# Optimization experiments

Hardware: AMD Instinct MI355X
Metric: run time of the kernel (lower is better)

The kernel has to match this reference:

```python
import jax, jax.numpy as jnp
import numpy as np

D_MODEL = 1024
NUM_HEADS = 16
D_K = D_MODEL // NUM_HEADS
B, S = 1, 4096


def setup_inputs() -> dict:
    key = jax.random.key(0)
    ks = jax.random.split(key, 11)
    std = 1.0 / np.sqrt(D_MODEL)
    def lin(k):
        kw, kb = jax.random.split(k)
        W = jax.random.uniform(kw, (D_MODEL, D_MODEL), jnp.float32, -std, std)
        b = jax.random.uniform(kb, (D_MODEL,), jnp.float32, -std, std)
        return W, b
    Wq, bq = lin(ks[0]); Wk, bk = lin(ks[1]); Wv, bv = lin(ks[2]); Wo, bo = lin(ks[3])
    q = jax.random.normal(ks[4], (B, S, D_MODEL), jnp.float32)
    k = jax.random.normal(ks[5], (B, S, D_MODEL), jnp.float32)
    v = jax.random.normal(ks[6], (B, S, D_MODEL), jnp.float32)
    return {"q": q, "k": k, "v": v,
            "Wq": Wq, "bq": bq, "Wk": Wk, "bk": bk,
            "Wv": Wv, "bv": bv, "Wo": Wo, "bo": bo}


def reference(q, k, v, Wq, bq, Wk, bk, Wv, bv, Wo, bo):
    Bq, Sq, _ = q.shape
    # Linear projections (torch Linear: x @ W.T + b)
    def split_heads(x):
        return x.reshape(Bq, -1, NUM_HEADS, D_K).transpose(0, 2, 1, 3)  # [B,H,S,Dk]
    query = split_heads(q @ Wq.T + bq)
    key_ = split_heads(k @ Wk.T + bk)
    value = split_heads(v @ Wv.T + bv)
    scores = jnp.einsum('bhsd,bhtd->bhst', query, key_) / jnp.sqrt(jnp.float32(D_K))
    attn = jax.nn.softmax(scores, axis=-1)  # [B,H,S,S]
    ctx = jnp.einsum('bhst,bhtd->bhsd', attn, value)
    ctx = ctx.transpose(0, 2, 1, 3).reshape(Bq, Sq, NUM_HEADS * D_K)
    return ctx @ Wo.T + bo
```

## Files before the change

kernel.cpp:

```cpp
#include <hip/hip_runtime.h>
#include <cstdint>
#include <cstddef>

#define S_LEN 4096
#define DMODEL 1024
#define NHEADS 16
#define DK 64
#define ACT (S_LEN * DMODEL)
#define WELE (DMODEL * DMODEL)

typedef __bf16 bf16;
typedef bf16  bf16x2 __attribute__((ext_vector_type(2)));
typedef bf16  bf16x4 __attribute__((ext_vector_type(4)));
typedef bf16  bf16x8 __attribute__((ext_vector_type(8)));
typedef float f32x4  __attribute__((ext_vector_type(4)));
typedef float f32x16 __attribute__((ext_vector_type(16)));
typedef unsigned int uint32x4v __attribute__((ext_vector_type(4)));

__device__ __forceinline__ void async16(const void* g, void* l) {
    __builtin_amdgcn_global_load_lds(
        (__attribute__((address_space(1))) void*)(uintptr_t)g,
        (__attribute__((address_space(3))) void*)(uintptr_t)l,
        16, 0, 0);
}

__device__ __forceinline__ float fast_exp2(float x) {
#if __has_builtin(__builtin_amdgcn_exp2f)
    return __builtin_amdgcn_exp2f(x);
#else
    return exp2f(x);
#endif
}

__device__ __forceinline__ unsigned pk2(float a, float b) {
    bf16x2 t; t[0] = (bf16)a; t[1] = (bf16)b;
    return __builtin_bit_cast(unsigned, t);
}

__device__ __forceinline__ void pl32swap(unsigned &a, unsigned &b) {
    asm volatile("v_permlane32_swap_b32 %0, %1" : "+v"(a), "+v"(b));
}

__device__ __forceinline__ bf16x8 mkfrag(unsigned w0, unsigned w1, unsigned w2, unsigned w3) {
    uint32x4v u = { w0, w1, w2, w3 };
    return __builtin_bit_cast(bf16x8, u);
}

__global__ void __launch_bounds__(256) cvt7(
    const float* a0, const float* a1, const float* a2,
    const float* w0, const float* w1, const float* w2, const float* w3,
    bf16* oa0, bf16* oa1, bf16* oa2,
    bf16* ow0, bf16* ow1, bf16* ow2, bf16* ow3,
    int nA, int nB)
{
    const float* s; bf16* d; int n4;
    switch (blockIdx.y) {
        case 0: s = a0; d = oa0; n4 = nA; break;
        case 1: s = a1; d = oa1; n4 = nA; break;
        case 2: s = a2; d = oa2; n4 = nA; break;
        case 3: s = w0; d = ow0; n4 = nB; break;
        case 4: s = w1; d = ow1; n4 = nB; break;
        case 5: s = w2; d = ow2; n4 = nB; break;
        default: s = w3; d = ow3; n4 = nB; break;
    }
    int i = blockIdx.x * 256 + threadIdx.x;
    if (i < n4) {
        float4 v = ((const float4*)s)[i];
        bf16x4 r = { (bf16)v.x, (bf16)v.y, (bf16)v.z, (bf16)v.w };
        ((bf16x4*)d)[i] = r;
    }
}

__device__ __forceinline__ void gemm_compute_128(
    const bf16* As, const bf16* Bs, f32x4 (&acc)[4][4],
    int wm, int wn, int l16, int quad)
{
    bf16x8 af[4], bfr[4];
#pragma unroll
    for (int i = 0; i < 4; ++i)
        af[i] = *(const bf16x8*)&As[(wm + i * 16 + l16) * 32 + quad * 8];
#pragma unroll
    for (int i = 0; i < 4; ++i)
        bfr[i] = *(const bf16x8*)&Bs[(wn + i * 16 + l16) * 32 + quad * 8];
#pragma unroll
    for (int mi = 0; mi < 4; ++mi)
#pragma unroll
        for (int ni = 0; ni < 4; ++ni)
            acc[mi][ni] = __builtin_amdgcn_mfma_f32_16x16x32_bf16(
                af[mi], bfr[ni], acc[mi][ni], 0, 0, 0);
}

__device__ __forceinline__ void gemm_core_bk64(
    const bf16* __restrict__ A, const bf16* __restrict__ B,
    bf16* As, bf16* Bs, f32x4 (&acc)[4][4],
    int m0, int n0, int wm, int wn, int K)
{
    const int tid  = threadIdx.x;
    const int wave = tid >> 6;
    const int lane = tid & 63;
    const int quad = lane >> 4;
    const int l16  = lane & 15;

    const int srow = tid >> 2;
    const int scol = (tid & 3) * 8;
    const bf16* Ag = A + (size_t)(m0 + srow) * K + scol;
    const bf16* Bg = B + (size_t)(n0 + srow) * K + scol;
    char* lA = (char*)As + wave * 1024;
    char* lB = (char*)Bs + wave * 1024;

    for (int k0 = 0; k0 < K; k0 += 64) {
        async16(Ag,                       lA);
        async16(Ag + (size_t)64 * K,      lA + 4096);
        async16(Ag + 32,                  lA + 8192);
        async16(Ag + 32 + (size_t)64 * K, lA + 12288);
        async16(Bg,                       lB);
        async16(Bg + (size_t)64 * K,      lB + 4096);
        async16(Bg + 32,                  lB + 8192);
        async16(Bg + 32 + (size_t)64 * K, lB + 12288);
        Ag += 64; Bg += 64;
        __syncthreads();

        gemm_compute_128(As,        Bs,        acc, wm, wn, l16, quad);
        gemm_compute_128(As + 4096, Bs + 4096, acc, wm, wn, l16, quad);
        __syncthreads();
    }
}

__global__ void __launch_bounds__(256) proj_qkv(
    const bf16* __restrict__ Xq, const bf16* __restrict__ Wq, const float* __restrict__ bq, bf16* __restrict__ Qo,
    const bf16* __restrict__ Xk, const bf16* __restrict__ Wk, const float* __restrict__ bk, bf16* __restrict__ Ko,
    const bf16* __restrict__ Xv, const bf16* __restrict__ Wv, const float* __restrict__ bv, bf16* __restrict__ Vo,
    float qscale)
{
    __shared__ __align__(16) bf16 As[2 * 128 * 32];
    __shared__ __align__(16) bf16 Bs[2 * 128 * 32];

    const int which = blockIdx.z;
    const bf16*  A    = (which == 0) ? Xq : (which == 1) ? Xk : Xv;
    const bf16*  Bw   = (which == 0) ? Wq : (which == 1) ? Wk : Wv;
    const float* bias = (which == 0) ? bq : (which == 1) ? bk : bv;
    const float  scale = (which == 0) ? qscale : 1.0f;

    const int tid  = threadIdx.x;
    const int wave = tid >> 6;
    const int lane = tid & 63;
    const int quad = lane >> 4;
    const int l16  = lane & 15;
    const int m0 = blockIdx.x * 128;
    const int n0 = blockIdx.y * 128;
    const int wm = (wave & 1) * 64;
    const int wn = (wave >> 1) * 64;

    f32x4 acc[4][4] = {};
    gemm_core_bk64(A, Bw, As, Bs, acc, m0, n0, wm, wn, DMODEL);

    if (which < 2) {
        bf16* out = (which == 0) ? Qo : Ko;
#pragma unroll
        for (int mi = 0; mi < 4; ++mi)
#pragma unroll
            for (int ni = 0; ni < 4; ++ni) {
                const int n = n0 + wn + ni * 16 + l16;
                const float bn = bias[n];
                const int dk = n & 63;
                const int cc = dk >> 3, ee = dk & 7;
                const size_t hb = (size_t)(n >> 6) * S_LEN * DK;
#pragma unroll
                for (int r = 0; r < 4; ++r) {
                    const int m = m0 + wm + mi * 16 + quad * 4 + r;
                    const int pdk = ((cc ^ (m & 7)) << 3) | ee;
                    out[hb + (size_t)m * DK + pdk] = (bf16)((acc[mi][ni][r] + bn) * scale);
                }
            }
    } else {
#pragma unroll
        for (int mi = 0; mi < 4; ++mi)
#pragma unroll
            for (int ni = 0; ni < 4; ++ni) {
                const int n = n0 + wn + ni * 16 + l16;
                const float bn = bias[n];
                const int dk = n & 63;
                const size_t hb = (size_t)(n >> 6) * (64 * S_LEN);
                const int mbase = m0 + wm + mi * 16 + quad * 4;
                const int T  = mbase >> 6;
                const int tt = mbase & 63;
                const int pos = (((tt >> 3) ^ (dk & 7)) << 3) | (tt & 7);
                bf16x4 r4;
#pragma unroll
                for (int r = 0; r < 4; ++r) r4[r] = (bf16)(acc[mi][ni][r] + bn);
                *(bf16x4*)&Vo[hb + (size_t)T * 4096 + dk * 64 + pos] = r4;
            }
    }
}

__global__ void __launch_bounds__(256) gemm_out(
    const bf16* __restrict__ A, const bf16* __restrict__ Bw,
    const float* __restrict__ bias, float* __restrict__ out)
{
    __shared__ __align__(16) bf16 As[64 * 32];
    __shared__ __align__(16) bf16 Bs[128 * 32];

    const int tid  = threadIdx.x;
    const int wave = tid >> 6;
    const int lane = tid & 63;
    const int quad = lane >> 4;
    const int l16  = lane & 15;
    const int m0 = blockIdx.x * 64;
    const int n0 = blockIdx.y * 128;
    const int wm = (wave & 1) * 32;
    const int wn = (wave >> 1) * 64;

    const int srow = tid >> 2;
    const int scol = (tid & 3) * 8;
    const bf16* Ag  = A  + (size_t)(m0 + srow) * DMODEL + scol;
    const bf16* Bg  = Bw + (size_t)(n0 + srow) * DMODEL + scol;
    const bf16* Bg2 = Bg + (size_t)64 * DMODEL;

    f32x4 acc[2][4] = {};
    for (int k0 = 0; k0 < DMODEL; k0 += 32) {
        async16(Ag,  (char*)As + wave * 1024);
        async16(Bg,  (char*)Bs + wave * 1024);
        async16(Bg2, (char*)Bs + 4096 + wave * 1024);
        Ag += 32; Bg += 32; Bg2 += 32;
        __syncthreads();

        bf16x8 af[2], bfr[4];
#pragma unroll
        for (int i = 0; i < 2; ++i)
            af[i] = *(const bf16x8*)&As[(wm + i * 16 + l16) * 32 + quad * 8];
#pragma unroll
        for (int i = 0; i < 4; ++i)
            bfr[i] = *(const bf16x8*)&Bs[(wn + i * 16 + l16) * 32 + quad * 8];

#pragma unroll
        for (int mi = 0; mi < 2; ++mi)
#pragma unroll
            for (int ni = 0; ni < 4; ++ni)
                acc[mi][ni] = __builtin_amdgcn_mfma_f32_16x16x32_bf16(
                    af[mi], bfr[ni], acc[mi][ni], 0, 0, 0);
        __syncthreads();
    }

#pragma unroll
    for (int mi = 0; mi < 2; ++mi)
#pragma unroll
        for (int ni = 0; ni < 4; ++ni) {
            const int n = n0 + wn + ni * 16 + l16;
            const float bn = bias[n];
#pragma unroll
            for (int r = 0; r < 4; ++r) {
                const int m = m0 + wm + mi * 16 + quad * 4 + r;
                out[(size_t)m * DMODEL + n] = acc[mi][ni][r] + bn;
            }
        }
}

__global__ void __launch_bounds__(512) flash_attn(
    const bf16* __restrict__ Q, const bf16* __restrict__ Kh,
    const bf16* __restrict__ Vt, bf16* __restrict__ ctx)
{
    __shared__ __align__(16) bf16 Qs[256 * 64];
    __shared__ __align__(16) bf16 Ks[3][64 * 64];
    __shared__ __align__(16) bf16 Vs[3][64 * 64];

    const int tid  = threadIdx.x;
    const int wave = tid >> 6;
    const int lane = tid & 63;
    const int l31  = lane & 31;
    const int hi   = lane >> 5;
    const int x7   = lane & 7;
    const int s0 = blockIdx.x * 256;
    const int h  = blockIdx.y;

    const bf16* Kg = Kh + (size_t)h * S_LEN * DK + tid * 8;
    const bf16* Vg = Vt + (size_t)h * (64 * S_LEN) + tid * 8;

    {
        const bf16* Qg = Q + (size_t)h * S_LEN * DK + (size_t)s0 * DK + tid * 8;
#pragma unroll
        for (int j = 0; j < 4; ++j)
            async16(Qg + j * 4096, (char*)Qs + j * 8192 + wave * 1024);
    }
    async16(Kg, (char*)Ks + wave * 1024);
    async16(Vg, (char*)Vs + wave * 1024);
    Kg += 4096; Vg += 4096;
    async16(Kg, (char*)Ks + 8192 + wave * 1024);
    async16(Vg, (char*)Vs + 8192 + wave * 1024);
    Kg += 4096; Vg += 4096;
    asm volatile("s_waitcnt vmcnt(2)" ::: "memory");
    __builtin_amdgcn_s_barrier();
    __builtin_amdgcn_sched_barrier(0);

    bf16x8 qf[4];
    {
        const bf16* qb = &Qs[(wave * 32 + l31) * 64];
#pragma unroll
        for (int ks = 0; ks < 4; ++ks)
            qf[ks] = *(const bf16x8*)(qb + ((((ks << 1) + hi) ^ x7) << 3));
    }

    f32x16 od[2] = {};
    float lsum = 0.0f;

    auto compute = [&](int cb) {
        const bf16* Kc = &Ks[cb][0];
        const bf16* Vc = &Vs[cb][0];

        f32x16 st[2] = {};
        __builtin_amdgcn_s_setprio(1);
#pragma unroll
        for (int tt = 0; tt < 2; ++tt) {
            const bf16* kb = &Kc[(tt * 32 + l31) * 64];
#pragma unroll
            for (int ks = 0; ks < 4; ++ks) {
                bf16x8 kf = *(const bf16x8*)(kb + ((((ks << 1) + hi) ^ x7) << 3));
                st[tt] = __builtin_amdgcn_mfma_f32_32x32x16_bf16(kf, qf[ks], st[tt], 0, 0, 0);
            }
        }
        __builtin_amdgcn_s_setprio(0);

        bf16x8 pf[4];
#pragma unroll
        for (int tt = 0; tt < 2; ++tt) {
            float p[16];
#pragma unroll
            for (int r = 0; r < 16; ++r) {
                p[r] = fast_exp2(st[tt][r]);
                lsum += p[r];
            }
#pragma unroll
            for (int w = 0; w < 2; ++w) {
                const int G = w * 8;
                unsigned A0 = pk2(p[G + 0], p[G + 1]);
                unsigned A1 = pk2(p[G + 2], p[G + 3]);
                unsigned B0 = pk2(p[G + 4], p[G + 5]);
                unsigned B1 = pk2(p[G + 6], p[G + 7]);
                pl32swap(A0, B0);
                pl32swap(A1, B1);
                pf[tt * 2 + w] = mkfrag(A0, A1, B0, B1);
            }
        }

        __builtin_amdgcn_s_setprio(1);
#pragma unroll
        for (int dd = 0; dd < 2; ++dd) {
            const bf16* vb = &Vc[(dd * 32 + l31) * 64];
#pragma unroll
            for (int ks = 0; ks < 4; ++ks) {
                bf16x8 vf = *(const bf16x8*)(vb + ((((ks << 1) + hi) ^ x7) << 3));
                od[dd] = __builtin_amdgcn_mfma_f32_32x32x16_bf16(vf, pf[ks], od[dd], 0, 0, 0);
            }
        }
        __builtin_amdgcn_s_setprio(0);
    };

    int cur = 0;
    for (int it = 0; it < 62; ++it) {
        int nb = cur + 2; if (nb >= 3) nb -= 3;
        async16(Kg, (char*)Ks + nb * 8192 + wave * 1024);
        async16(Vg, (char*)Vs + nb * 8192 + wave * 1024);
        Kg += 4096; Vg += 4096;

        compute(cur);

        asm volatile("s_waitcnt vmcnt(2)" ::: "memory");
        __builtin_amdgcn_s_barrier();
        __builtin_amdgcn_sched_barrier(0);
        cur = (cur + 1 == 3) ? 0 : cur + 1;
    }
    compute(cur);
    asm volatile("s_waitcnt vmcnt(0)" ::: "memory");
    __builtin_amdgcn_s_barrier();
    __builtin_amdgcn_sched_barrier(0);
    cur = (cur + 1 == 3) ? 0 : cur + 1;
    compute(cur);

    lsum += __shfl_xor(lsum, 32);
    const float rinv = 1.0f / lsum;
    const int s = s0 + wave * 32 + l31;
#pragma unroll
    for (int dd = 0; dd < 2; ++dd)
#pragma unroll
        for (int g = 0; g < 4; ++g) {
            bf16x4 r4;
#pragma unroll
            for (int r = 0; r < 4; ++r)
                r4[r] = (bf16)(od[dd][g * 4 + r] * rinv);
            *(bf16x4*)&ctx[(size_t)s * DMODEL + h * DK + dd * 32 + g * 8 + hi * 4] = r4;
        }
}

extern "C" void kernel_launch(void* const* d_in, const int* in_sizes, int n_in,
                              void* d_out, int out_size, void* d_ws, size_t ws_size,
                              hipStream_t stream)
{
    (void)in_sizes; (void)n_in; (void)out_size; (void)ws_size;
    const float* q  = (const float*)d_in[0];
    const float* k  = (const float*)d_in[1];
    const float* v  = (const float*)d_in[2];
    const float* Wq = (const float*)d_in[3];
    const float* bq = (const float*)d_in[4];
    const float* Wk = (const float*)d_in[5];
    const float* bk = (const float*)d_in[6];
    const float* Wv = (const float*)d_in[7];
    const float* bv = (const float*)d_in[8];
    const float* Wo = (const float*)d_in[9];
    const float* bo = (const float*)d_in[10];

    bf16* Xq  = (bf16*)d_ws;
    bf16* Xk  = Xq  + ACT;
    bf16* Xv  = Xk  + ACT;
    bf16* Wqb = Xv  + ACT;
    bf16* Wkb = Wqb + WELE;
    bf16* Wvb = Wkb + WELE;
    bf16* Wob = Wvb + WELE;
    bf16* Qh  = Wob + WELE;
    bf16* Kh  = Qh  + ACT;
    bf16* Vt  = Kh  + ACT;
    bf16* CTX = Vt  + ACT;

    cvt7<<<dim3(ACT / 4 / 256, 7), 256, 0, stream>>>(
        q, k, v, Wq, Wk, Wv, Wo,
        Xq, Xk, Xv, Wqb, Wkb, Wvb, Wob, ACT / 4, WELE / 4);

    const float qscale = 0.125f * 1.4426950408889634f;
    proj_qkv<<<dim3(S_LEN / 128, DMODEL / 128, 3), 256, 0, stream>>>(
        Xq, Wqb, bq, Qh, Xk, Wkb, bk, Kh, Xv, Wvb, bv, Vt, qscale);

    flash_attn<<<dim3(S_LEN / 256, NHEADS), 512, 0, stream>>>(Qh, Kh, Vt, CTX);

    gemm_out<<<dim3(S_LEN / 64, DMODEL / 128), 256, 0, stream>>>(CTX, Wob, bo, (float*)d_out);
}
```

Measured before the change: 254.9 us.

## Split attention KV range across two blocks and merge with atomics

The flash attention grid gains a z dimension of 2, so each block processes half the key/value sequence. Each block atomically adds its unnormalized output accumulator and row sums into fp32 workspace buffers. A new combine kernel then divides by the summed row sums and writes bf16 context. The aim is to double the block count, since the old grid had only 256 large blocks, and so improve CU utilisation. The cost is an extra memset, float atomics over the full activation, and an extra pass. The merge is only correct if both halves use a consistent softmax max reference.

```diff
diff --git a/kernel.cpp b/kernel.cpp
--- a/kernel.cpp
+++ b/kernel.cpp
@@ -257,7 +257,8 @@
 
 __global__ void __launch_bounds__(512) flash_attn(
     const bf16* __restrict__ Q, const bf16* __restrict__ Kh,
-    const bf16* __restrict__ Vt, bf16* __restrict__ ctx)
+    const bf16* __restrict__ Vt, float* __restrict__ accO,
+    float* __restrict__ lsums)
 {
     __shared__ __align__(16) bf16 Qs[256 * 64];
     __shared__ __align__(16) bf16 Ks[3][64 * 64];
@@ -271,9 +272,10 @@
     const int x7   = lane & 7;
     const int s0 = blockIdx.x * 256;
     const int h  = blockIdx.y;
-
-    const bf16* Kg = Kh + (size_t)h * S_LEN * DK + tid * 8;
-    const bf16* Vg = Vt + (size_t)h * (64 * S_LEN) + tid * 8;
+    const int z  = blockIdx.z;
+
+    const bf16* Kg = Kh + (size_t)h * S_LEN * DK + (size_t)z * 2048 * DK + tid * 8;
+    const bf16* Vg = Vt + (size_t)h * (64 * S_LEN) + (size_t)z * 32 * 4096 + tid * 8;
 
     {
         const bf16* Qg = Q + (size_t)h * S_LEN * DK + (size_t)s0 * DK + tid * 8;
@@ -355,7 +357,7 @@
     };
 
     int cur = 0;
-    for (int it = 0; it < 62; ++it) {
+    for (int it = 0; it < 30; ++it) {
         int nb = cur + 2; if (nb >= 3) nb -= 3;
         async16(Kg, (char*)Ks + nb * 8192 + wave * 1024);
         async16(Vg, (char*)Vs + nb * 8192 + wave * 1024);
@@ -375,19 +377,28 @@
     cur = (cur + 1 == 3) ? 0 : cur + 1;
     compute(cur);
 
-    lsum += __shfl_xor(lsum, 32);
-    const float rinv = 1.0f / lsum;
     const int s = s0 + wave * 32 + l31;
+    atomicAdd(&lsums[s * NHEADS + h], lsum);
+    float* base = accO + (size_t)s * DMODEL + h * DK;
 #pragma unroll
     for (int dd = 0; dd < 2; ++dd)
 #pragma unroll
-        for (int g = 0; g < 4; ++g) {
-            bf16x4 r4;
+        for (int g = 0; g < 4; ++g)
 #pragma unroll
             for (int r = 0; r < 4; ++r)
-                r4[r] = (bf16)(od[dd][g * 4 + r] * rinv);
-            *(bf16x4*)&ctx[(size_t)s * DMODEL + h * DK + dd * 32 + g * 8 + hi * 4] = r4;
-        }
+                atomicAdd(&base[dd * 32 + g * 8 + hi * 4 + r], od[dd][g * 4 + r]);
+}
+
+__global__ void __launch_bounds__(256) combine(
+    const float* __restrict__ accO, const float* __restrict__ lsums,
+    bf16* __restrict__ ctx)
+{
+    const int idx = blockIdx.x * 256 + threadIdx.x;
+    float4 a = ((const float4*)accO)[idx];
+    const float rinv = 1.0f / lsums[idx >> 4];
+    bf16x4 r = { (bf16)(a.x * rinv), (bf16)(a.y * rinv),
+                 (bf16)(a.z * rinv), (bf16)(a.w * rinv) };
+    ((bf16x4*)ctx)[idx] = r;
 }
 
 extern "C" void kernel_launch(void* const* d_in, const int* in_sizes, int n_in,
@@ -419,6 +430,9 @@
     bf16* Vt  = Kh  + ACT;
     bf16* CTX = Vt  + ACT;
 
+    float* accO  = (float*)d_ws;
+    float* lsums = accO + ACT;
+
     cvt7<<<dim3(ACT / 4 / 256, 7), 256, 0, stream>>>(
         q, k, v, Wq, Wk, Wv, Wo,
         Xq, Xk, Xv, Wqb, Wkb, Wvb, Wob, ACT / 4, WELE / 4);
@@ -427,7 +441,12 @@
     proj_qkv<<<dim3(S_LEN / 128, DMODEL / 128, 3), 256, 0, stream>>>(
         Xq, Wqb, bq, Qh, Xk, Wkb, bk, Kh, Xv, Wvb, bv, Vt, qscale);
 
-    flash_attn<<<dim3(S_LEN / 256, NHEADS), 512, 0, stream>>>(Qh, Kh, Vt, CTX);
+    hipMemsetAsync(accO, 0, (size_t)(ACT + S_LEN * NHEADS) * sizeof(float), stream);
+
+    flash_attn<<<dim3(S_LEN / 256, NHEADS, 2), 512, 0, stream>>>(
+        Qh, Kh, Vt, accO, lsums);
+
+    combine<<<dim3(ACT / 4 / 256), 256, 0, stream>>>(accO, lsums, CTX);
 
     gemm_out<<<dim3(S_LEN / 64, DMODEL / 128), 256, 0, stream>>>(CTX, Wob, bo, (float*)d_out);
 }
```

New measurement: 468.2 us. 83.7% more time.
